# Optimization experiments

Hardware: AMD Instinct MI355X
Metric: run time of the kernel (lower is better)

## Reference

```python
import jax, jax.numpy as jnp
import numpy as np

N_NODES = 50000


def gcn_conv(x, W, src, dst, n):
    # PyG GCNConv(bias=False): h = x @ W, then symmetric-normalized
    # aggregation over A + I (self-loops added, normalize=True).
    h = x @ W  # [N, F_out]
    loop = jnp.arange(n, dtype=src.dtype)
    s = jnp.concatenate([src, loop])  # source nodes (messages come from x_j = h[s])
    d = jnp.concatenate([dst, loop])  # target nodes (aggregation index)
    ones = jnp.ones(s.shape[0], dtype=h.dtype)
    deg = jax.ops.segment_sum(ones, d, num_segments=n)  # in-degree incl. self-loop
    dinv = jnp.where(deg > 0, jax.lax.rsqrt(deg), 0.0)
    norm = dinv[s] * dinv[d]  # per-edge D^-1/2 A_hat D^-1/2 weight
    msgs = h[s] * norm[:, None]  # gather + scale
    return jax.ops.segment_sum(msgs, d, num_segments=n)  # scatter-add


def setup_inputs() -> dict:
    key = jax.random.key(0)
    k1, k2, k3, k4 = jax.random.split(key, 4)
    x = jax.random.normal(k1, (N_NODES, 256), dtype=jnp.float32)
    edge_index = jax.random.randint(k2, (2, 1600000), 0, N_NODES, dtype=jnp.int64)
    # glorot-scale weights
    W1 = jax.random.normal(k3, (256, 256), dtype=jnp.float32) * (1.0 / np.sqrt(256))
    W3 = jax.random.normal(k4, (256, 64), dtype=jnp.float32) * (1.0 / np.sqrt(256))
    return {"x": x, "edge_index": edge_index, "W1": W1, "W3": W3}


def reference(x, edge_index, W1, W3):
    n = x.shape[0]
    src, dst = edge_index[0], edge_index[1]
    h = jax.nn.relu(gcn_conv(x, W1, src, dst, n))
    h = jax.nn.relu(gcn_conv(h, W3, src, dst, n))
    return h
```

## Files before the change

### kernel.cpp

```cpp
#include <hip/hip_runtime.h>
#include <cstdint>
#include <cstddef>


#define NPART 128

__device__ __forceinline__ float bf2f(unsigned short u) {
    union { unsigned int i; float f; } c; c.i = ((unsigned int)u) << 16; return c.f;
}
__device__ __forceinline__ unsigned short f2bf(float f) {
    union { float f; unsigned int i; } c; c.f = f;
    unsigned int r = c.i + 0x7fffu + ((c.i >> 16) & 1u);
    return (unsigned short)(r >> 16);
}

__global__ __launch_bounds__(256) void wcvt2_kernel(const float* __restrict__ W1,
                                                    const float* __restrict__ W3,
                                                    unsigned short* __restrict__ W1t,
                                                    unsigned short* __restrict__ W3t) {
    int idx = blockIdx.x * 256 + threadIdx.x;
    if (idx < 256 * 256) {
        int nn = idx >> 8, kk = idx & 255;
        W1t[idx] = f2bf(W1[kk * 256 + nn]);
    } else if (idx < 256 * 256 + 64 * 256) {
        int j = idx - 256 * 256;
        int nn = j >> 8, kk = j & 255;
        W3t[j] = f2bf(W3[kk * 64 + nn]);
    }
}


__global__ __launch_bounds__(256) void part_hist(const int* __restrict__ dst, int E, int NB,
                                                 int* __restrict__ blockhist) {
    __shared__ int lh[1024];
    for (int t = threadIdx.x; t < NB; t += 256) lh[t] = 0;
    __syncthreads();
    const int per = (E + NPART - 1) / NPART;
    const int beg = blockIdx.x * per;
    const int end = min(E, beg + per);
    for (int i = beg + threadIdx.x; i < end; i += 256)
        atomicAdd(&lh[dst[i] >> 6], 1);
    __syncthreads();
    for (int t = threadIdx.x; t < NB; t += 256)
        blockhist[blockIdx.x * NB + t] = lh[t];
}

__global__ __launch_bounds__(1024) void part_scan(const int* __restrict__ blockhist,
                                                  int* __restrict__ bofs,
                                                  int* __restrict__ bbase, int NB) {
    __shared__ int wsum[16];
    const int t = threadIdx.x;
    const int lane = t & 63;
    int tot = 0;
    if (t < NB) {
        #pragma unroll 4
        for (int k = 0; k < NPART; ++k) tot += blockhist[k * NB + t];
    }
    int x = tot;
    #pragma unroll
    for (int off = 1; off < 64; off <<= 1) {
        int q = __shfl_up(x, off);
        if (lane >= off) x += q;
    }
    if (lane == 63) wsum[t >> 6] = x;
    __syncthreads();
    if (t < 64) {
        int y = (t < 16) ? wsum[t] : 0;
        #pragma unroll
        for (int off = 1; off < 16; off <<= 1) {
            int q = __shfl_up(y, off);
            if (lane >= off) y += q;
        }
        if (t < 16) wsum[t] = y;
    }
    __syncthreads();
    int excl = ((t >> 6) ? wsum[(t >> 6) - 1] : 0) + x - tot;
    if (t < NB) {
        bofs[t] = excl;
        if (t == NB - 1) bofs[NB] = excl + tot;
        int run = excl;
        for (int k = 0; k < NPART; ++k) {
            int c = blockhist[k * NB + t];
            bbase[k * NB + t] = run;
            run += c;
        }
    }
}

__global__ __launch_bounds__(256) void part_scatter(const int* __restrict__ src,
                                                    const int* __restrict__ dst,
                                                    const int* __restrict__ bbase,
                                                    unsigned int* __restrict__ words,
                                                    int E, int NB) {
    __shared__ int lbase[1024];
    for (int t = threadIdx.x; t < NB; t += 256) lbase[t] = bbase[blockIdx.x * NB + t];
    __syncthreads();
    const int per = (E + NPART - 1) / NPART;
    const int beg = blockIdx.x * per;
    const int end = min(E, beg + per);
    for (int i = beg + threadIdx.x; i < end; i += 256) {
        int d = dst[i];
        int off = atomicAdd(&lbase[d >> 6], 1);
        words[off] = ((unsigned)src[i] << 6) | (unsigned)(d & 63);
    }
}

__global__ __launch_bounds__(256) void bucket_build(const unsigned int* __restrict__ words,
                                                    const int* __restrict__ bofs,
                                                    int* __restrict__ rowptr,
                                                    float* __restrict__ dinv,
                                                    int* __restrict__ csr, int n) {
    const int b = blockIdx.x;
    const int node0 = b << 6;
    __shared__ int ldeg[64], lcur[64];
    if (threadIdx.x < 64) ldeg[threadIdx.x] = 0;
    __syncthreads();
    const int beg = bofs[b], end = bofs[b + 1];
    for (int i = beg + threadIdx.x; i < end; i += 256)
        atomicAdd(&ldeg[words[i] & 63u], 1);
    __syncthreads();
    if (threadIdx.x < 64) {
        const int lane = threadIdx.x;
        int v = ldeg[lane];
        int x = v;
        #pragma unroll
        for (int off = 1; off < 64; off <<= 1) {
            int q = __shfl_up(x, off);
            if (lane >= off) x += q;
        }
        int excl = x - v;
        int node = node0 + lane;
        if (node < n) {
            rowptr[node] = beg + excl;
            dinv[node] = rsqrtf((float)(v + 1));
        }
        lcur[lane] = beg + excl;
        if (b == (int)gridDim.x - 1 && lane == 0) rowptr[n] = end;
    }
    __syncthreads();
    for (int i = beg + threadIdx.x; i < end; i += 256) {
        unsigned int w = words[i];
        int pos = atomicAdd(&lcur[w & 63u], 1);
        csr[pos] = (int)(w >> 6);
    }
}

template<int BN, int WM, int WN, bool AF32, bool CTILED>
__global__ __launch_bounds__(256) void mfma_gemm(const void* __restrict__ Av,
                                                 const unsigned short* __restrict__ Bt,
                                                 const float* __restrict__ dinvp,
                                                 unsigned short* __restrict__ C,
                                                 int M, int N, int K) {
    constexpr int BM = 128, BK = 64;
    constexpr int KP = 72;
    constexpr int WTM = BM / WM;
    constexpr int WTN = BN / WN;
    constexpr int MF = WTM / 16;
    constexpr int NF = WTN / 16;
    __shared__ unsigned short As[BM][KP];
    __shared__ unsigned short Bs[BN][KP];
    const int tid = threadIdx.x;
    const int wid = tid >> 6;
    const int lane = tid & 63;
    const int wr = wid / WN;
    const int wc = wid % WN;
    const int bm = blockIdx.y * BM;
    const int bn = blockIdx.x * BN;
    const int l15 = lane & 15;
    const int lg = lane >> 4;

    using bf16x8 = __attribute__((ext_vector_type(8))) short;
    using f32x4  = __attribute__((ext_vector_type(4))) float;
    f32x4 acc[MF][NF] = {};

    for (int k0 = 0; k0 < K; k0 += BK) {
        #pragma unroll
        for (int it = 0; it < (BM * BK / 8) / 256; ++it) {
            int v = tid + 256 * it;
            int row = v >> 3;
            int oct = v & 7;
            uint4 val = make_uint4(0, 0, 0, 0);
            int gr = bm + row;
            if (gr < M) {
                if (AF32) {
                    const float* A32 = (const float*)Av;
                    float4 f0 = *(const float4*)(A32 + (size_t)gr * K + k0 + oct * 8);
                    float4 f1 = *(const float4*)(A32 + (size_t)gr * K + k0 + oct * 8 + 4);
                    union { unsigned short u[8]; uint4 v4; } pk;
                    pk.u[0] = f2bf(f0.x); pk.u[1] = f2bf(f0.y);
                    pk.u[2] = f2bf(f0.z); pk.u[3] = f2bf(f0.w);
                    pk.u[4] = f2bf(f1.x); pk.u[5] = f2bf(f1.y);
                    pk.u[6] = f2bf(f1.z); pk.u[7] = f2bf(f1.w);
                    val = pk.v4;
                } else {
                    const unsigned short* Ab = (const unsigned short*)Av;
                    val = *(const uint4*)(Ab + (size_t)gr * K + k0 + oct * 8);
                }
            }
            *(uint4*)(&As[row][oct * 8]) = val;
        }
        #pragma unroll
        for (int it = 0; it < (BN * BK / 8) / 256; ++it) {
            int v = tid + 256 * it;
            int row = v >> 3;
            int oct = v & 7;
            uint4 val = *(const uint4*)(Bt + (size_t)(bn + row) * K + k0 + oct * 8);
            *(uint4*)(&Bs[row][oct * 8]) = val;
        }
        __syncthreads();
        #pragma unroll
        for (int kk = 0; kk < 2; ++kk) {
            bf16x8 af[MF], bfr[NF];
            #pragma unroll
            for (int m = 0; m < MF; ++m)
                af[m] = *(const bf16x8*)(&As[wr * WTM + m * 16 + l15][kk * 32 + lg * 8]);
            #pragma unroll
            for (int nf = 0; nf < NF; ++nf)
                bfr[nf] = *(const bf16x8*)(&Bs[wc * WTN + nf * 16 + l15][kk * 32 + lg * 8]);
            #pragma unroll
            for (int m = 0; m < MF; ++m)
                #pragma unroll
                for (int nf = 0; nf < NF; ++nf)
                    acc[m][nf] = __builtin_amdgcn_mfma_f32_16x16x32_bf16(
                        af[m], bfr[nf], acc[m][nf], 0, 0, 0);
        }
        __syncthreads();
    }
    #pragma unroll
    for (int m = 0; m < MF; ++m) {
        #pragma unroll
        for (int j = 0; j < 4; ++j) {
            int row = bm + wr * WTM + m * 16 + lg * 4 + j;
            if (row < M) {
                float s = dinvp[row];
                #pragma unroll
                for (int nf = 0; nf < NF; ++nf) {
                    int col = bn + wc * WTN + nf * 16 + l15;
                    unsigned short v = f2bf(acc[m][nf][j] * s);
                    if (CTILED)
                        C[((size_t)(col >> 5) * M + row) * 32 + (col & 31)] = v;
                    else
                        C[(size_t)row * N + col] = v;
                }
            }
        }
    }
}

__global__ __launch_bounds__(256) void agg256_tiled(
        const unsigned short* __restrict__ hst, const int* __restrict__ rowptr,
        const int* __restrict__ csr, const float* __restrict__ dinv,
        unsigned short* __restrict__ out, int n) {
    const int t = blockIdx.x & 7;
    const int g = blockIdx.x >> 3;
    const int wv = threadIdx.x >> 6;
    const int half = (threadIdx.x >> 5) & 1;
    const int c = threadIdx.x & 31;
    const int d = g * 8 + wv * 2 + half;
    if (d >= n) return;
    const unsigned short* slice = hst + (size_t)t * n * 32;

    float acc = bf2f(slice[(size_t)d * 32 + c]);
    const int beg = rowptr[d];
    const int deg = rowptr[d + 1] - beg;

    int k = 0;
    for (; k + 4 <= deg; k += 4) {
        int s0 = csr[beg + k];
        int s1 = csr[beg + k + 1];
        int s2 = csr[beg + k + 2];
        int s3 = csr[beg + k + 3];
        float v0 = bf2f(slice[(size_t)s0 * 32 + c]);
        float v1 = bf2f(slice[(size_t)s1 * 32 + c]);
        float v2 = bf2f(slice[(size_t)s2 * 32 + c]);
        float v3 = bf2f(slice[(size_t)s3 * 32 + c]);
        acc += (v0 + v1) + (v2 + v3);
    }
    for (; k < deg; ++k)
        acc += bf2f(slice[(size_t)csr[beg + k] * 32 + c]);

    out[(size_t)d * 256 + t * 32 + c] = f2bf(fmaxf(dinv[d] * acc, 0.f));
}

__global__ __launch_bounds__(256) void aggregate64_kernel(
        const unsigned short* __restrict__ hs, const int* __restrict__ rowptr,
        const int* __restrict__ csr, const float* __restrict__ dinv,
        float* __restrict__ out, int n) {
    const int d = blockIdx.x;
    const int tid = threadIdx.x;
    const int wid = tid >> 6;
    const int lane = tid & 63;
    const int beg = rowptr[d];
    const int end = rowptr[d + 1];

    float acc = 0.f;
    if (wid == 0) acc = bf2f(hs[(size_t)d * 64 + lane]);

    __shared__ unsigned int soff[256];
    const char* hb = (const char*)hs;
    for (int k0 = beg; k0 < end; k0 += 256) {
        int cnt = min(256, end - k0);
        if (tid < cnt) soff[tid] = (unsigned)csr[k0 + tid] * 128u;
        __syncthreads();
        #pragma unroll 8
        for (int e = wid; e < cnt; e += 4) {
            unsigned short t = *(const unsigned short*)(hb + soff[e] + lane * 2);
            acc += bf2f(t);
        }
        __syncthreads();
    }

    __shared__ float part[3][64];
    if (wid > 0) part[wid - 1][lane] = acc;
    __syncthreads();
    if (wid == 0) {
        acc += part[0][lane] + part[1][lane] + part[2][lane];
        out[(size_t)d * 64 + lane] = fmaxf(dinv[d] * acc, 0.f);
    }
}


static inline size_t align256(size_t v) { return (v + 255) & ~(size_t)255; }

extern "C" void kernel_launch(void* const* d_in, const int* in_sizes, int n_in,
                              void* d_out, int out_size, void* d_ws, size_t ws_size,
                              hipStream_t stream) {
    const float* x  = (const float*)d_in[0];
    const int*   ei = (const int*)d_in[1];
    const float* W1 = (const float*)d_in[2];
    const float* W3 = (const float*)d_in[3];

    const int n = in_sizes[0] / 256;
    const int E = in_sizes[1] / 2;
    const int NB = (n + 63) >> 6;
    const int* src = ei;
    const int* dst = ei + E;

    char* w = (char*)d_ws;
    auto alloc = [&](size_t bytes) { char* p = w; w += align256(bytes); return p; };
    unsigned short* hs1t = (unsigned short*)alloc((size_t)n * 256 * 2);
    unsigned short* a1   = (unsigned short*)alloc((size_t)n * 256 * 2);
    unsigned short* hs2  = (unsigned short*)alloc((size_t)n * 64 * 2);
    unsigned short* W1t  = (unsigned short*)alloc(256 * 256 * 2);
    unsigned short* W3t  = (unsigned short*)alloc(64 * 256 * 2);
    float* dinv          = (float*)alloc((size_t)n * 4);
    int*   rowptr        = (int*)alloc((size_t)(n + 1) * 4);
    int*   csr           = (int*)alloc((size_t)E * 4);
    unsigned int* words  = (unsigned int*)alloc((size_t)E * 4);
    int*   blockhist     = (int*)alloc((size_t)NPART * NB * 4);
    int*   bbase         = (int*)alloc((size_t)NPART * NB * 4);
    int*   bofs          = (int*)alloc((size_t)(NB + 1) * 4);
    float* out           = (float*)d_out;

    wcvt2_kernel<<<(256 * 256 + 64 * 256 + 255) / 256, 256, 0, stream>>>(W1, W3, W1t, W3t);

    part_hist<<<NPART, 256, 0, stream>>>(dst, E, NB, blockhist);
    part_scan<<<1, 1024, 0, stream>>>(blockhist, bofs, bbase, NB);
    part_scatter<<<NPART, 256, 0, stream>>>(src, dst, bbase, words, E, NB);
    bucket_build<<<NB, 256, 0, stream>>>(words, bofs, rowptr, dinv, csr, n);

    {
        dim3 grid(1, (n + 127) / 128);
        mfma_gemm<256, 2, 2, true, true><<<grid, 256, 0, stream>>>(x, W1t, dinv, hs1t, n, 256, 256);
        int ngrp = (n + 7) / 8;
        agg256_tiled<<<ngrp * 8, 256, 0, stream>>>(hs1t, rowptr, csr, dinv, a1, n);
    }
    {
        dim3 grid(1, (n + 127) / 128);
        mfma_gemm<64, 4, 1, false, false><<<grid, 256, 0, stream>>>(a1, W3t, dinv, hs2, n, 64, 256);
        aggregate64_kernel<<<n, 256, 0, stream>>>(hs2, rowptr, csr, dinv, out, n);
    }
}
```

Measured before the change: 369.9 us.

## Process eight neighbors per wave with vectorized loads in tiled 256-wide aggregation

The 256-wide aggregation kernel now gives each 64-lane wave one destination node. The wave is split into eight groups of eight lanes, and each group gathers a different neighbor's 32-column slice with 8-byte ushort4 loads. Partial sums are combined with xor shuffles and written back as packed bf16. This is meant to put more independent gather requests in flight and use wider loads. In exchange, each wave handles half as many nodes, the grid doubles in size, and the shuffle reduction adds overhead.

Result: faster. 361.6 us (-2.2%).

```diff
diff --git a/kernel.cpp b/kernel.cpp
--- a/kernel.cpp
+++ b/kernel.cpp
@@ -252,34 +252,56 @@
         const int* __restrict__ csr, const float* __restrict__ dinv,
         unsigned short* __restrict__ out, int n) {
     const int t = blockIdx.x & 7;
-    const int g = blockIdx.x >> 3;
+    const int g4 = blockIdx.x >> 3;
     const int wv = threadIdx.x >> 6;
-    const int half = (threadIdx.x >> 5) & 1;
-    const int c = threadIdx.x & 31;
-    const int d = g * 8 + wv * 2 + half;
+    const int lane = threadIdx.x & 63;
+    const int grp = lane >> 3;
+    const int j = lane & 7;
+    const int d = g4 * 4 + wv;
     if (d >= n) return;
-    const unsigned short* slice = hst + (size_t)t * n * 32;
-
-    float acc = bf2f(slice[(size_t)d * 32 + c]);
+    const char* sb = (const char*)(hst + (size_t)t * n * 32);
+
+    float a0 = 0.f, a1 = 0.f, a2 = 0.f, a3 = 0.f;
+    if (grp == 0) {
+        ushort4 v = *(const ushort4*)(sb + (size_t)d * 64 + j * 8);
+        a0 = bf2f(v.x); a1 = bf2f(v.y); a2 = bf2f(v.z); a3 = bf2f(v.w);
+    }
+
     const int beg = rowptr[d];
     const int deg = rowptr[d + 1] - beg;
-
     int k = 0;
-    for (; k + 4 <= deg; k += 4) {
-        int s0 = csr[beg + k];
-        int s1 = csr[beg + k + 1];
-        int s2 = csr[beg + k + 2];
-        int s3 = csr[beg + k + 3];
-        float v0 = bf2f(slice[(size_t)s0 * 32 + c]);
-        float v1 = bf2f(slice[(size_t)s1 * 32 + c]);
-        float v2 = bf2f(slice[(size_t)s2 * 32 + c]);
-        float v3 = bf2f(slice[(size_t)s3 * 32 + c]);
-        acc += (v0 + v1) + (v2 + v3);
-    }
-    for (; k < deg; ++k)
-        acc += bf2f(slice[(size_t)csr[beg + k] * 32 + c]);
-
-    out[(size_t)d * 256 + t * 32 + c] = f2bf(fmaxf(dinv[d] * acc, 0.f));
+    #pragma unroll 2
+    for (; k + 8 <= deg; k += 8) {
+        int s = csr[beg + k + grp];
+        ushort4 v = *(const ushort4*)(sb + (size_t)s * 64 + j * 8);
+        a0 += bf2f(v.x); a1 += bf2f(v.y);
+        a2 += bf2f(v.z); a3 += bf2f(v.w);
+    }
+    if (k < deg) {
+        if (k + grp < deg) {
+            int s = csr[beg + k + grp];
+            ushort4 v = *(const ushort4*)(sb + (size_t)s * 64 + j * 8);
+            a0 += bf2f(v.x); a1 += bf2f(v.y);
+            a2 += bf2f(v.z); a3 += bf2f(v.w);
+        }
+    }
+
+    #pragma unroll
+    for (int off = 8; off < 64; off <<= 1) {
+        a0 += __shfl_xor(a0, off);
+        a1 += __shfl_xor(a1, off);
+        a2 += __shfl_xor(a2, off);
+        a3 += __shfl_xor(a3, off);
+    }
+    if (grp == 0) {
+        const float wd = dinv[d];
+        union { unsigned short u[4]; uint2 v; } pk;
+        pk.u[0] = f2bf(fmaxf(wd * a0, 0.f));
+        pk.u[1] = f2bf(fmaxf(wd * a1, 0.f));
+        pk.u[2] = f2bf(fmaxf(wd * a2, 0.f));
+        pk.u[3] = f2bf(fmaxf(wd * a3, 0.f));
+        *(uint2*)(out + (size_t)d * 256 + t * 32 + j * 4) = pk.v;
+    }
 }
 
 __global__ __launch_bounds__(256) void aggregate64_kernel(
@@ -362,7 +384,7 @@
     {
         dim3 grid(1, (n + 127) / 128);
         mfma_gemm<256, 2, 2, true, true><<<grid, 256, 0, stream>>>(x, W1t, dinv, hs1t, n, 256, 256);
-        int ngrp = (n + 7) / 8;
+        int ngrp = (n + 3) / 4;
         agg256_tiled<<<ngrp * 8, 256, 0, stream>>>(hs1t, rowptr, csr, dinv, a1, n);
     }
     {
```
